# Performance work log

Measured on AMD Instinct MI355X. Metric: run time of the kernel, lower is better.

The kernel has to match this reference:

```python
import jax, jax.numpy as jnp
import numpy as np

B, S, D = 4, 2048, 1024
H, E = 8, 128  # num_head, num_dim (per-head)

def setup_inputs() -> dict:
    key = jax.random.key(0)
    ks = jax.random.split(key, 8)
    scale_in = 1.0 / np.sqrt(D)
    return {
        "q": jax.random.normal(ks[0], (B, S, D), dtype=jnp.float32),
        "k": jax.random.normal(ks[1], (B, S, D), dtype=jnp.float32),
        "v": jax.random.normal(ks[2], (B, S, D), dtype=jnp.float32),
        "Wq": jax.random.normal(ks[3], (H, D, E), dtype=jnp.float32) * scale_in,
        "Wk": jax.random.normal(ks[4], (H, D, E), dtype=jnp.float32) * scale_in,
        "Wv": jax.random.normal(ks[5], (H, D, E), dtype=jnp.float32) * scale_in,
        "Wo": jax.random.normal(ks[6], (H * E, D), dtype=jnp.float32) * (1.0 / np.sqrt(H * E)),
        "bo": jnp.zeros((D,), dtype=jnp.float32),
    }

def reference(q, k, v, Wq, Wk, Wv, Wo, bo):
    dk = jnp.asarray(E, q.dtype) ** 0.5
    # per-head projections, all heads batched: [B,H,S,E]
    qh = jnp.einsum("bsd,hde->bhse", q, Wq)
    kh = jnp.einsum("bsd,hde->bhse", k, Wk)
    vh = jnp.einsum("bsd,hde->bhse", v, Wv)
    scores = jnp.einsum("bhse,bhte->bhst", qh / dk, kh)  # [B,H,S,S]
    attn = jax.nn.softmax(scores, axis=-1)
    zh = jnp.einsum("bhst,bhte->bhse", attn, vh)  # [B,H,S,E]
    # concat heads along feature dim (head order preserved): [B,S,H*E]
    z = jnp.transpose(zh, (0, 2, 1, 3)).reshape(B, S, H * E)
    return z @ Wo + bo
```

## Files before the change

kernel.cpp:

```cpp
#include <hip/hip_runtime.h>

#define B_ 4
#define S_ 2048
#define D_ 1024
#define H_ 8
#define E_ 128

typedef __bf16 bf16_t;
typedef __bf16 bf16x4 __attribute__((ext_vector_type(4)));
typedef __bf16 bf16x8 __attribute__((ext_vector_type(8)));
typedef float f32x4 __attribute__((ext_vector_type(4)));

#define MFMA16(a, b, c) __builtin_amdgcn_mfma_f32_16x16x32_bf16(a, b, c, 0, 0, 0)

#define LDP_ 64

__device__ __forceinline__ void load_lds16(const bf16_t* g, bf16_t* l) {
    __builtin_amdgcn_global_load_lds(
        (const __attribute__((address_space(1))) unsigned int*)g,
        (__attribute__((address_space(3))) unsigned int*)l,
        16, 0, 0);
}

__device__ __forceinline__ f32x4 zero4() {
    f32x4 z = {0.f, 0.f, 0.f, 0.f};
    return z;
}

__global__ __launch_bounds__(64) void detect_dtype(const unsigned int* __restrict__ q,
                                                   int* __restrict__ flag) {
    int lane = threadIdx.x;
    int cnt = 0;
    for (int i = lane; i < 4096; i += 64) {
        unsigned e = (q[i] >> 7) & 0xFFu;
        cnt += (e >= 110u && e <= 141u) ? 1 : 0;
    }
#pragma unroll
    for (int d = 32; d; d >>= 1) cnt += __shfl_down(cnt, d);
    if (lane == 0) *flag = (cnt > 2048) ? 1 : 0;
}

__global__ __launch_bounds__(256) void convert_bf16(const void* __restrict__ p0,
                                                    const void* __restrict__ p1,
                                                    const void* __restrict__ p2,
                                                    bf16_t* __restrict__ out,
                                                    const int* __restrict__ flagp) {
    const size_t QSZ = (size_t)B_ * H_ * S_ * E_;
    int z = blockIdx.z;
    const void* in = (z == 0) ? p0 : (z == 1) ? p1 : p2;
    bf16_t* o = out + (size_t)z * QSZ;
    int isb = *flagp;
    size_t i = ((size_t)blockIdx.x * 256 + threadIdx.x) * 8;
    if (isb) {
        *(bf16x8*)(o + i) = *(const bf16x8*)((const bf16_t*)in + i);
    } else {
        const float* p = (const float*)in + i;
        f32x4 lo = *(const f32x4*)p;
        f32x4 hi = *(const f32x4*)(p + 4);
        bf16x8 v;
#pragma unroll
        for (int j = 0; j < 4; j++) { v[j] = (bf16_t)lo[j]; v[4 + j] = (bf16_t)hi[j]; }
        *(bf16x8*)(o + i) = v;
    }
}

__global__ __launch_bounds__(256) void transpose_any(const void* __restrict__ p0,
                                                     const void* __restrict__ p1,
                                                     const void* __restrict__ p2,
                                                     bf16_t* __restrict__ out,
                                                     int R, int C,
                                                     const int* __restrict__ flagp) {
    __shared__ bf16_t tile[32][33];
    int isb = *flagp;
    int bz = blockIdx.z;
    int sel = bz >> 3, sub = bz & 7;
    const void* in = (sel == 0) ? p0 : (sel == 1) ? p1 : p2;
    const bf16_t* inb16 = (const bf16_t*)in + (size_t)sub * R * C;
    const float*  inb32 = (const float*)in + (size_t)sub * R * C;
    bf16_t* outb = out + (size_t)bz * R * C;
    int tx = threadIdx.x & 31, ty = threadIdx.x >> 5;
    int r0 = blockIdx.y * 32, c0 = blockIdx.x * 32;
#pragma unroll
    for (int i = 0; i < 4; i++) {
        size_t idx = (size_t)(r0 + ty + i * 8) * C + c0 + tx;
        tile[ty + i * 8][tx] = isb ? inb16[idx] : (bf16_t)inb32[idx];
    }
    __syncthreads();
#pragma unroll
    for (int i = 0; i < 4; i++)
        outb[(size_t)(c0 + ty + i * 8) * R + r0 + tx] = tile[tx][ty + i * 8];
}

__global__ __launch_bounds__(256) void proj_gemm(const bf16_t* __restrict__ Abase,
                                                 int useZ,
                                                 const bf16_t* __restrict__ WtBase,
                                                 bf16_t* __restrict__ OutBase,
                                                 float qscale, int z0) {
    __shared__ __align__(16) bf16_t Alds[128 * 64];
    __shared__ __align__(16) bf16_t Blds[128 * 64];
    const size_t WSZ = (size_t)H_ * E_ * D_;
    const size_t QSZ = (size_t)B_ * H_ * S_ * E_;
    int z = z0 + blockIdx.z;
    const bf16_t* A = Abase + (useZ ? (size_t)z * QSZ : 0);
    const bf16_t* Bt = WtBase + (size_t)z * WSZ + (size_t)blockIdx.y * E_ * D_;
    bf16_t* Out = OutBase + (size_t)z * QSZ;
    int vmode = (z == 2);
    float oscale = (z == 0) ? qscale : 1.0f;

    int m0 = blockIdx.x * 128;
    int h = blockIdx.y;
    int t = threadIdx.x;
    int w = t >> 6, lane = t & 63;
    int quad = lane >> 4, ln = lane & 15;
    int wm = (w >> 1) * 64, wn = (w & 1) * 64;

    f32x4 acc[4][4];
#pragma unroll
    for (int i = 0; i < 4; i++)
#pragma unroll
        for (int j = 0; j < 4; j++) acc[i][j] = zero4();

    for (int k0 = 0; k0 < D_; k0 += 64) {
#pragma unroll
        for (int j = 0; j < 4; j++) {
            int base = j * 256 + w * 64;
            int G = base + lane;
            int r = G >> 3, sl = G & 7;
            int c = sl ^ (r & 7);
            load_lds16(A + (size_t)(m0 + r) * D_ + k0 + c * 8, Alds + (size_t)base * 8);
            load_lds16(Bt + (size_t)r * D_ + k0 + c * 8, Blds + (size_t)base * 8);
        }
        asm volatile("s_waitcnt vmcnt(0)" ::: "memory");
        __syncthreads();

        const bf16_t* Xsrc = vmode ? Blds : Alds;
        const bf16_t* Ysrc = vmode ? Alds : Blds;
#pragma unroll
        for (int ks = 0; ks < 2; ks++) {
            bf16x8 xf[4], yf[4];
#pragma unroll
            for (int mt = 0; mt < 4; mt++) {
                int row = wm + mt * 16 + ln;
                xf[mt] = *(const bf16x8*)(Xsrc + (size_t)row * 64 +
                                          (((ks << 2) + quad) ^ (row & 7)) * 8);
            }
#pragma unroll
            for (int nt = 0; nt < 4; nt++) {
                int row = wn + nt * 16 + ln;
                yf[nt] = *(const bf16x8*)(Ysrc + (size_t)row * 64 +
                                          (((ks << 2) + quad) ^ (row & 7)) * 8);
            }
#pragma unroll
            for (int mt = 0; mt < 4; mt++)
#pragma unroll
                for (int nt = 0; nt < 4; nt++)
                    acc[mt][nt] = MFMA16(xf[mt], yf[nt], acc[mt][nt]);
        }
        __syncthreads();
    }

#pragma unroll
    for (int mt = 0; mt < 4; mt++) {
#pragma unroll
        for (int nt = 0; nt < 4; nt++) {
#pragma unroll
            for (int r = 0; r < 4; r++) {
                int M = wm + mt * 16 + quad * 4 + r;
                int N = wn + nt * 16 + ln;
                float v = acc[mt][nt][r] * oscale;
                size_t idx;
                if (vmode == 0) {
                    int g = m0 + M;
                    int b = g >> 11, s = g & 2047;
                    idx = ((size_t)((b * H_ + h) * S_ + s)) * E_ + N;
                } else {
                    int g = m0 + N;
                    int b = g >> 11, s = g & 2047;
                    idx = ((size_t)((b * H_ + h) * E_ + M)) * S_ + s;
                }
                Out[idx] = (bf16_t)v;
            }
        }
    }
}

__global__ __launch_bounds__(512, 2) void flash_attn(const bf16_t* __restrict__ Qh,
                                                     const bf16_t* __restrict__ Kh,
                                                     const bf16_t* __restrict__ Vt,
                                                     bf16_t* __restrict__ Z) {
    __shared__ __align__(16) bf16_t Klds[64 * 128];
    __shared__ __align__(16) bf16_t Vlds[128 * 64];
    __shared__ __align__(16) bf16_t Plds[8 * 32 * LDP_];
    int bh = blockIdx.y;
    int qt = blockIdx.x;
    const bf16_t* Qbh = Qh + (size_t)bh * S_ * E_;
    const bf16_t* Kbh = Kh + (size_t)bh * S_ * E_;
    const bf16_t* Vbh = Vt + (size_t)bh * E_ * S_;
    int t = threadIdx.x, w = t >> 6, lane = t & 63;
    int quad = lane >> 4, ln = lane & 15;
    bf16_t* Pw = Plds + w * 32 * LDP_;
    int psw = (ln & 7) << 3;

    bf16x8 qf[2][4];
#pragma unroll
    for (int mt = 0; mt < 2; mt++)
#pragma unroll
        for (int ks = 0; ks < 4; ks++)
            qf[mt][ks] = *(const bf16x8*)(Qbh + (size_t)(qt * 256 + w * 32 + mt * 16 + ln) * E_ +
                                          ks * 32 + quad * 8);

    f32x4 oacc[2][8];
#pragma unroll
    for (int mt = 0; mt < 2; mt++)
#pragma unroll
        for (int nt = 0; nt < 8; nt++) oacc[mt][nt] = zero4();
    float rsum[2] = {0.f, 0.f};

    const bf16_t* kfp[4][4];
#pragma unroll
    for (int nt = 0; nt < 4; nt++)
#pragma unroll
        for (int ks = 0; ks < 4; ks++)
            kfp[nt][ks] = Klds + (size_t)(nt * 16 + ln) * 128 +
                          (((ks * 4 + quad) ^ ln) & 15) * 8;
    const bf16_t* vfp[2][8];
#pragma unroll
    for (int ks = 0; ks < 2; ks++)
#pragma unroll
        for (int nt = 0; nt < 8; nt++) {
            int n = nt * 16 + ln;
            vfp[ks][nt] = Vlds + (size_t)n * 64 + (((ks * 4 + quad) ^ n) & 7) * 8;
        }
    const bf16_t* pfp[2][2];
#pragma unroll
    for (int ks = 0; ks < 2; ks++)
#pragma unroll
        for (int mt = 0; mt < 2; mt++)
            pfp[ks][mt] = Pw + (((mt * 16 + ln) * LDP_ + ks * 32 + quad * 8) ^ psw);
    bf16_t* pwp[4][2];
#pragma unroll
    for (int nt = 0; nt < 4; nt++)
#pragma unroll
        for (int mt = 0; mt < 2; mt++)
            pwp[nt][mt] = Pw + (((mt * 16 + ln) * LDP_ + nt * 16 + quad * 4) ^ psw);

    bf16_t* kst[2];
    bf16_t* vst[2];
    const bf16_t* gkp[2];
    const bf16_t* gvp[2];
#pragma unroll
    for (int j = 0; j < 2; j++) {
        int G = j * 512 + t;
        int rK = G >> 4, cK = (G & 15) ^ (rK & 15);
        int rV = G >> 3, cV = (G & 7) ^ (rV & 7);
        kst[j] = Klds + G * 8;
        vst[j] = Vlds + G * 8;
        gkp[j] = Kbh + rK * E_ + cK * 8;
        gvp[j] = Vbh + rV * S_ + cV * 8;
    }

    bf16x8 gK[2], gV[2];
#pragma unroll
    for (int j = 0; j < 2; j++) {
        gK[j] = *(const bf16x8*)gkp[j];
        gV[j] = *(const bf16x8*)gvp[j];
    }

    const int NT = S_ / 64;
    for (int kt = 0; kt < NT; kt++) {
#pragma unroll
        for (int j = 0; j < 2; j++) {
            *(bf16x8*)kst[j] = gK[j];
            *(bf16x8*)vst[j] = gV[j];
        }
        __syncthreads();

        int kadv = (kt + 1 < NT) ? 64 * E_ : 0;
        int vadv = (kt + 1 < NT) ? 64 : 0;
#pragma unroll
        for (int j = 0; j < 2; j++) {
            gkp[j] += kadv;
            gvp[j] += vadv;
            gK[j] = *(const bf16x8*)gkp[j];
            gV[j] = *(const bf16x8*)gvp[j];
        }
        __builtin_amdgcn_sched_barrier(0);

#pragma unroll
        for (int nt = 0; nt < 4; nt++) {
            f32x4 sacc[2];
            sacc[0] = zero4();
            sacc[1] = zero4();
            __builtin_amdgcn_s_setprio(1);
#pragma unroll
            for (int ks = 0; ks < 4; ks++) {
                bf16x8 kf = *(const bf16x8*)kfp[nt][ks];
#pragma unroll
                for (int mt = 0; mt < 2; mt++) sacc[mt] = MFMA16(kf, qf[mt][ks], sacc[mt]);
            }
            __builtin_amdgcn_s_setprio(0);
#pragma unroll
            for (int mt = 0; mt < 2; mt++) {
                bf16x4 pk;
#pragma unroll
                for (int r = 0; r < 4; r++) {
                    float p = exp2f(sacc[mt][r] - 18.0f);
                    rsum[mt] += p;
                    pk[r] = (bf16_t)p;
                }
                *(bf16x4*)pwp[nt][mt] = pk;
            }
        }

        asm volatile("s_waitcnt lgkmcnt(0)" ::: "memory");

        __builtin_amdgcn_s_setprio(1);
#pragma unroll
        for (int ks = 0; ks < 2; ks++) {
            bf16x8 pf[2], vf[8];
#pragma unroll
            for (int mt = 0; mt < 2; mt++) pf[mt] = *(const bf16x8*)pfp[ks][mt];
#pragma unroll
            for (int nt = 0; nt < 8; nt++) vf[nt] = *(const bf16x8*)vfp[ks][nt];
#pragma unroll
            for (int mt = 0; mt < 2; mt++)
#pragma unroll
                for (int nt = 0; nt < 8; nt++)
                    oacc[mt][nt] = MFMA16(pf[mt], vf[nt], oacc[mt][nt]);
        }
        __builtin_amdgcn_s_setprio(0);
        __syncthreads();
    }

    float linv[2][4];
#pragma unroll
    for (int mt = 0; mt < 2; mt++) {
        float v = rsum[mt];
        v += __shfl_xor(v, 16);
        v += __shfl_xor(v, 32);
#pragma unroll
        for (int r = 0; r < 4; r++) linv[mt][r] = 1.0f / __shfl(v, quad * 4 + r);
    }

    int b = bh >> 3, h = bh & 7;
#pragma unroll
    for (int mt = 0; mt < 2; mt++) {
#pragma unroll
        for (int nt = 0; nt < 8; nt++) {
#pragma unroll
            for (int r = 0; r < 4; r++) {
                int s = qt * 256 + w * 32 + mt * 16 + quad * 4 + r;
                int col = h * E_ + nt * 16 + ln;
                Z[((size_t)(b * S_ + s)) * (H_ * E_) + col] =
                    (bf16_t)(oacc[mt][nt][r] * linv[mt][r]);
            }
        }
    }
}

__global__ __launch_bounds__(256) void final_gemm(const bf16_t* __restrict__ A,
                                                  const bf16_t* __restrict__ Bt,
                                                  const void* __restrict__ bias,
                                                  void* __restrict__ Out,
                                                  const int* __restrict__ flagp) {
    __shared__ __align__(16) bf16_t Alds[128 * 64];
    __shared__ __align__(16) bf16_t Blds[128 * 64];
    int isb = *flagp;
    int m0 = blockIdx.x * 128;
    int n0 = blockIdx.y * 128;
    int t = threadIdx.x;
    int w = t >> 6, lane = t & 63;
    int quad = lane >> 4, ln = lane & 15;
    int wm = (w >> 1) * 64, wn = (w & 1) * 64;

    f32x4 acc[4][4];
#pragma unroll
    for (int i = 0; i < 4; i++)
#pragma unroll
        for (int j = 0; j < 4; j++) acc[i][j] = zero4();

    for (int k0 = 0; k0 < D_; k0 += 64) {
#pragma unroll
        for (int j = 0; j < 4; j++) {
            int base = j * 256 + w * 64;
            int G = base + lane;
            int r = G >> 3, sl = G & 7;
            int c = sl ^ (r & 7);
            load_lds16(A + (size_t)(m0 + r) * (H_ * E_) + k0 + c * 8, Alds + (size_t)base * 8);
            load_lds16(Bt + (size_t)(n0 + r) * (H_ * E_) + k0 + c * 8, Blds + (size_t)base * 8);
        }
        asm volatile("s_waitcnt vmcnt(0)" ::: "memory");
        __syncthreads();

#pragma unroll
        for (int ks = 0; ks < 2; ks++) {
            bf16x8 af[4], bfr[4];
#pragma unroll
            for (int mt = 0; mt < 4; mt++) {
                int row = wm + mt * 16 + ln;
                af[mt] = *(const bf16x8*)(Alds + (size_t)row * 64 +
                                          (((ks << 2) + quad) ^ (row & 7)) * 8);
            }
#pragma unroll
            for (int nt = 0; nt < 4; nt++) {
                int row = wn + nt * 16 + ln;
                bfr[nt] = *(const bf16x8*)(Blds + (size_t)row * 64 +
                                           (((ks << 2) + quad) ^ (row & 7)) * 8);
            }
#pragma unroll
            for (int mt = 0; mt < 4; mt++)
#pragma unroll
                for (int nt = 0; nt < 4; nt++)
                    acc[mt][nt] = MFMA16(af[mt], bfr[nt], acc[mt][nt]);
        }
        __syncthreads();
    }

#pragma unroll
    for (int mt = 0; mt < 4; mt++) {
#pragma unroll
        for (int nt = 0; nt < 4; nt++) {
#pragma unroll
            for (int r = 0; r < 4; r++) {
                int grow = m0 + wm + mt * 16 + quad * 4 + r;
                int col = n0 + wn + nt * 16 + ln;
                float bv = isb ? (float)((const bf16_t*)bias)[col]
                               : ((const float*)bias)[col];
                float v = acc[mt][nt][r] + bv;
                size_t idx = (size_t)grow * D_ + col;
                if (isb) ((bf16_t*)Out)[idx] = (bf16_t)v;
                else     ((float*)Out)[idx] = v;
            }
        }
    }
}

extern "C" void kernel_launch(void* const* d_in, const int* in_sizes, int n_in,
                              void* d_out, int out_size, void* d_ws, size_t ws_size,
                              hipStream_t stream) {
    const void* q  = d_in[0];
    const void* k  = d_in[1];
    const void* v  = d_in[2];
    const void* Wq = d_in[3];
    const void* Wk = d_in[4];
    const void* Wv = d_in[5];
    const void* Wo = d_in[6];
    const void* bo = d_in[7];

    int* flag = (int*)d_ws;
    bf16_t* arena = (bf16_t*)((char*)d_ws + 256);
    const size_t WSZ = (size_t)H_ * E_ * D_;
    const size_t QSZ = (size_t)B_ * H_ * S_ * E_;
    bf16_t* wqt = arena;
    bf16_t* wot = wqt + 3 * WSZ;

    const size_t bigBytes = 256 + 2 * (4 * WSZ + 6 * QSZ);
    const bool big = (ws_size >= bigBytes);

    dim3 blk(256);
    const float qscale = 0.08838834764831845f * 1.44269504088896340f;

    detect_dtype<<<dim3(1), dim3(64), 0, stream>>>((const unsigned int*)q, flag);
    transpose_any<<<dim3(4, 32, 24), blk, 0, stream>>>(Wq, Wk, Wv, wqt, D_, E_, flag);
    transpose_any<<<dim3(32, 32, 1), blk, 0, stream>>>(Wo, Wo, Wo, wot, H_ * E_, D_, flag);

    if (big) {
        bf16_t* conv0 = wot + WSZ;
        bf16_t* Qh = conv0 + 3 * QSZ;
        bf16_t* Kh = Qh + QSZ;
        bf16_t* Vt = Kh + QSZ;
        bf16_t* Z  = conv0;

        convert_bf16<<<dim3(4096, 1, 3), blk, 0, stream>>>(q, k, v, conv0, flag);
        proj_gemm<<<dim3(64, 8, 3), blk, 0, stream>>>(conv0, 1, wqt, Qh, qscale, 0);
        flash_attn<<<dim3(8, 32), dim3(512), 0, stream>>>(Qh, Kh, Vt, Z);
        final_gemm<<<dim3(64, 8), blk, 0, stream>>>(Z, wot, bo, d_out, flag);
    } else {
        bf16_t* conv = wot + WSZ;
        bf16_t* Qh = conv + QSZ;
        bf16_t* Kh = Qh + QSZ;
        bf16_t* Vt = Kh + QSZ;
        bf16_t* Z  = conv;

        convert_bf16<<<dim3(4096, 1, 1), blk, 0, stream>>>(q, q, q, conv, flag);
        proj_gemm<<<dim3(64, 8, 1), blk, 0, stream>>>(conv, 0, wqt, Qh, qscale, 0);
        convert_bf16<<<dim3(4096, 1, 1), blk, 0, stream>>>(k, k, k, conv, flag);
        proj_gemm<<<dim3(64, 8, 1), blk, 0, stream>>>(conv, 0, wqt, Qh, qscale, 1);
        convert_bf16<<<dim3(4096, 1, 1), blk, 0, stream>>>(v, v, v, conv, flag);
        proj_gemm<<<dim3(64, 8, 1), blk, 0, stream>>>(conv, 0, wqt, Qh, qscale, 2);
        flash_attn<<<dim3(8, 32), dim3(512), 0, stream>>>(Qh, Kh, Vt, Z);
        final_gemm<<<dim3(64, 8), blk, 0, stream>>>(Z, wot, bo, d_out, flag);
    }
}
```

Measured before the change: 365.8 us.

## Prefetch next A tile into registers in projection and output GEMMs

In both the QKV projection GEMM and the output-projection GEMM, the A operand tile for the next k-step is loaded into registers right after the barrier, so the load overlaps the MFMA work on the current tile. At the top of the next iteration those registers are written to LDS instead of using direct global-to-LDS loads, and the swizzle indices are precomputed once before the loop. The B tile still uses synchronous global-to-LDS loads, so only half of the memory latency is hidden. The change costs extra VGPRs, which may reduce occupancy, and adds LDS store instructions.

```diff
diff --git a/kernel.cpp b/kernel.cpp
--- a/kernel.cpp
+++ b/kernel.cpp
@@ -120,18 +120,35 @@
 #pragma unroll
         for (int j = 0; j < 4; j++) acc[i][j] = zero4();
 
+    int jr[4], jc[4];
+#pragma unroll
+    for (int j = 0; j < 4; j++) {
+        int G = j * 256 + w * 64 + lane;
+        jr[j] = G >> 3;
+        jc[j] = (G & 7) ^ ((G >> 3) & 7);
+    }
+
+    bf16x8 aReg[4];
+#pragma unroll
+    for (int j = 0; j < 4; j++)
+        aReg[j] = *(const bf16x8*)(A + (size_t)(m0 + jr[j]) * D_ + jc[j] * 8);
+
     for (int k0 = 0; k0 < D_; k0 += 64) {
 #pragma unroll
-        for (int j = 0; j < 4; j++) {
-            int base = j * 256 + w * 64;
-            int G = base + lane;
-            int r = G >> 3, sl = G & 7;
-            int c = sl ^ (r & 7);
-            load_lds16(A + (size_t)(m0 + r) * D_ + k0 + c * 8, Alds + (size_t)base * 8);
-            load_lds16(Bt + (size_t)r * D_ + k0 + c * 8, Blds + (size_t)base * 8);
-        }
+        for (int j = 0; j < 4; j++)
+            load_lds16(Bt + (size_t)jr[j] * D_ + k0 + jc[j] * 8,
+                       Blds + (size_t)(j * 256 + w * 64) * 8);
+#pragma unroll
+        for (int j = 0; j < 4; j++)
+            *(bf16x8*)(Alds + (size_t)(j * 256 + w * 64 + lane) * 8) = aReg[j];
         asm volatile("s_waitcnt vmcnt(0)" ::: "memory");
         __syncthreads();
+
+        int k1 = (k0 + 64 < D_) ? k0 + 64 : k0;
+#pragma unroll
+        for (int j = 0; j < 4; j++)
+            aReg[j] = *(const bf16x8*)(A + (size_t)(m0 + jr[j]) * D_ + k1 + jc[j] * 8);
+        __builtin_amdgcn_sched_barrier(0);
 
         const bf16_t* Xsrc = vmode ? Blds : Alds;
         const bf16_t* Ysrc = vmode ? Alds : Blds;
@@ -379,18 +396,35 @@
 #pragma unroll
         for (int j = 0; j < 4; j++) acc[i][j] = zero4();
 
+    int jr[4], jc[4];
+#pragma unroll
+    for (int j = 0; j < 4; j++) {
+        int G = j * 256 + w * 64 + lane;
+        jr[j] = G >> 3;
+        jc[j] = (G & 7) ^ ((G >> 3) & 7);
+    }
+
+    bf16x8 aReg[4];
+#pragma unroll
+    for (int j = 0; j < 4; j++)
+        aReg[j] = *(const bf16x8*)(A + (size_t)(m0 + jr[j]) * (H_ * E_) + jc[j] * 8);
+
     for (int k0 = 0; k0 < D_; k0 += 64) {
 #pragma unroll
-        for (int j = 0; j < 4; j++) {
-            int base = j * 256 + w * 64;
-            int G = base + lane;
-            int r = G >> 3, sl = G & 7;
-            int c = sl ^ (r & 7);
-            load_lds16(A + (size_t)(m0 + r) * (H_ * E_) + k0 + c * 8, Alds + (size_t)base * 8);
-            load_lds16(Bt + (size_t)(n0 + r) * (H_ * E_) + k0 + c * 8, Blds + (size_t)base * 8);
-        }
+        for (int j = 0; j < 4; j++)
+            load_lds16(Bt + (size_t)(n0 + jr[j]) * (H_ * E_) + k0 + jc[j] * 8,
+                       Blds + (size_t)(j * 256 + w * 64) * 8);
+#pragma unroll
+        for (int j = 0; j < 4; j++)
+            *(bf16x8*)(Alds + (size_t)(j * 256 + w * 64 + lane) * 8) = aReg[j];
         asm volatile("s_waitcnt vmcnt(0)" ::: "memory");
         __syncthreads();
+
+        int k1 = (k0 + 64 < D_) ? k0 + 64 : k0;
+#pragma unroll
+        for (int j = 0; j < 4; j++)
+            aReg[j] = *(const bf16x8*)(A + (size_t)(m0 + jr[j]) * (H_ * E_) + k1 + jc[j] * 8);
+        __builtin_amdgcn_sched_barrier(0);
 
 #pragma unroll
         for (int ks = 0; ks < 2; ks++) {
```

New measurement: 362.7 us, median of 3. Within noise of the previous version (-0.8%).
